# Optimization experiments

Hardware: AMD Instinct MI355X
Metric: run time of the kernel (lower is better)

## Reference

```python
import jax, jax.numpy as jnp
import numpy as np

D = 1024      # hidden_size
FF = 4096     # ff_inner_dim = 4 * D
E = 8         # num_experts
K = 2         # moe_top_k
B, L = 4, 1024


def setup_inputs() -> dict:
    key = jax.random.key(0)
    ks = jax.random.split(key, 12)
    s = 0.02  # weight init scale
    return {
        "x": jax.random.normal(ks[0], (B, L, D), jnp.float32),
        "W_gate": jax.random.normal(ks[1], (D, E), jnp.float32) * s,
        "W1": jax.random.normal(ks[2], (E, D, FF), jnp.float32) * s,
        "b1": jnp.zeros((E, FF), jnp.float32),
        "W2": jax.random.normal(ks[3], (E, FF, D), jnp.float32) * s,
        "b2": jnp.zeros((E, D), jnp.float32),
        "Ws1": jax.random.normal(ks[4], (D, FF), jnp.float32) * s,
        "bs1": jnp.zeros((FF,), jnp.float32),
        "Ws2": jax.random.normal(ks[5], (FF, D), jnp.float32) * s,
        "bs2": jnp.zeros((D,), jnp.float32),
    }


def _gelu(h):
    # torch F.gelu default = exact (erf) gelu
    return jax.nn.gelu(h, approximate=False)


def reference(x, W_gate, W1, b1, W2, b2, Ws1, bs1, Ws2, bs2):
    Bx, Lx, Dx = x.shape
    xf = x.reshape(-1, Dx)                       # [T, D]
    logits = xf @ W_gate                         # [T, E]
    probs = jax.nn.softmax(logits, axis=-1)
    top_v, top_i = jax.lax.top_k(probs, K)       # [T, K]
    top_v = top_v / jnp.sum(top_v, axis=-1, keepdims=True)
    # dense combine weights: [T, E], zero for unselected experts
    combine = jnp.sum(jax.nn.one_hot(top_i, E, dtype=xf.dtype) * top_v[..., None], axis=1)

    out = jnp.zeros_like(xf)
    for e in range(E):  # fixed small expert loop, unrolled under jit
        h = _gelu(xf @ W1[e] + b1[e])            # [T, FF]
        out = out + combine[:, e:e + 1] * (h @ W2[e] + b2[e])

    shared = _gelu(xf @ Ws1 + bs1) @ Ws2 + bs2   # [T, D]
    return (out + shared).reshape(Bx, Lx, Dx)
```

## Files before the change

kernel.cpp:

```cpp
#include <hip/hip_runtime.h>
#include <hip/hip_bf16.h>

typedef unsigned short ushort_t;
typedef __attribute__((ext_vector_type(4))) float f32x4;
typedef __attribute__((ext_vector_type(8))) short bf16x8;
typedef __attribute__((ext_vector_type(8))) unsigned short us8;

#define T_TOK 4096
#define D_DIM 1024
#define FF_DIM 4096
#define NE 8
#define ESTRIDE 4194304L

__device__ __forceinline__ unsigned short f2bf(float f) {
  __hip_bfloat16 h = __float2bfloat16(f);
  return __builtin_bit_cast(unsigned short, h);
}
__device__ __forceinline__ float gelu_f(float v) {
  return 0.5f * v * (1.0f + erff(v * 0.70710678118654752440f));
}

__global__ void gate_kernel(const float* __restrict__ x, const float* __restrict__ Wg,
                            int* __restrict__ cnt, int* __restrict__ tok,
                            float* __restrict__ wof, int* __restrict__ rankof) {
  const int t = blockIdx.x;
  const int lane = threadIdx.x;
  const float* xr = x + (long)t * D_DIM;
  float acc[NE];
#pragma unroll
  for (int e = 0; e < NE; e++) acc[e] = 0.f;
#pragma unroll
  for (int i = 0; i < 16; i++) {
    int d = i * 64 + lane;
    float xv = xr[d];
    const float* wr = Wg + d * NE;
#pragma unroll
    for (int e = 0; e < NE; e++) acc[e] += xv * wr[e];
  }
#pragma unroll
  for (int off = 32; off > 0; off >>= 1) {
#pragma unroll
    for (int e = 0; e < NE; e++) acc[e] += __shfl_xor(acc[e], off, 64);
  }
  if (lane == 0) {
    int i0 = 0;
#pragma unroll
    for (int e = 1; e < NE; e++) if (acc[e] > acc[i0]) i0 = e;
    int i1 = -1;
#pragma unroll
    for (int e = 0; e < NE; e++) {
      if (e == i0) continue;
      if (i1 < 0 || acc[e] > acc[i1]) i1 = e;
    }
    float e1 = expf(acc[i1] - acc[i0]);
    float w0 = 1.f / (1.f + e1);
    float w1 = e1 * w0;
    int s0 = atomicAdd(&cnt[i0], 1);
    tok[i0 * T_TOK + s0] = t; wof[i0 * T_TOK + s0] = w0; rankof[i0 * T_TOK + s0] = 0;
    int s1 = atomicAdd(&cnt[i1], 1);
    tok[i1 * T_TOK + s1] = t; wof[i1 * T_TOK + s1] = w1; rankof[i1 * T_TOK + s1] = 1;
    tok[8 * T_TOK + t] = t; wof[8 * T_TOK + t] = 1.f; rankof[8 * T_TOK + t] = 0;
  }
}

__global__ void scan_kernel(int* cnt, int* base) {
  if (threadIdx.x == 0 && blockIdx.x == 0) {
    int s = 0;
    for (int e = 0; e < NE; e++) { base[e] = s; s += cnt[e]; }
    base[8] = s;
    cnt[8] = T_TOK;
  }
}

__global__ void build_queue_kernel(const int* __restrict__ cnt,
                                   unsigned int* __restrict__ q1,
                                   unsigned int* __restrict__ q2,
                                   int* __restrict__ nq) {
  const int e = blockIdx.x;
  int off1 = 0, off2 = 0, tot1 = 0, tot2 = 0, M = 0;
  for (int i = 0; i < 9; i++) {
    int c = (i == 8) ? T_TOK : cnt[i];
    int m = (c + 255) >> 8;
    if (i < e) { off1 += m * 16; off2 += m * 4; }
    if (i == e) M = m;
    tot1 += m * 16; tot2 += m * 4;
  }
  for (int i = threadIdx.x; i < M * 16; i += 256) {
    int my = i >> 4, nx = i & 15;
    int ms = my >> 1, mi = my & 1, ns = nx >> 2, ni = nx & 3;
    int h = M - ms * 2; if (h > 2) h = 2;
    int pos = ms * 32 + ns * (h * 4) + mi * 4 + ni;
    q1[off1 + pos] = ((unsigned)e << 16) | ((unsigned)my << 8) | (unsigned)nx;
  }
  for (int i = threadIdx.x; i < M * 4; i += 256) {
    int my = i >> 2, nx = i & 3;
    int pos = nx * M + my;
    q2[off2 + pos] = ((unsigned)e << 16) | ((unsigned)my << 8) | (unsigned)nx;
  }
  if (e == 0 && threadIdx.x == 0) { nq[0] = tot1; nq[1] = tot2; }
}

__global__ void cvt_x_kernel(const float* __restrict__ src, ushort_t* __restrict__ dst) {
  long i = ((long)blockIdx.x * 256 + threadIdx.x) * 8;
  float4 v0 = *(const float4*)(src + i);
  float4 v1 = *(const float4*)(src + i + 4);
  us8 o;
  o[0] = f2bf(v0.x); o[1] = f2bf(v0.y); o[2] = f2bf(v0.z); o[3] = f2bf(v0.w);
  o[4] = f2bf(v1.x); o[5] = f2bf(v1.y); o[6] = f2bf(v1.z); o[7] = f2bf(v1.w);
  *(us8*)(dst + i) = o;
}

__global__ void tcvt_kernel(const float* __restrict__ W, const float* __restrict__ Wsh,
                            ushort_t* __restrict__ dst, int R, int C) {
  const float* src = (blockIdx.z == 8) ? Wsh : (W + (long)blockIdx.z * R * C);
  ushort_t* d = dst + (long)blockIdx.z * R * C;
  const int r0 = blockIdx.y * 128, c0 = blockIdx.x * 64;
  __shared__ ushort_t tile[64][136];
  const int t = threadIdx.x;
#pragma unroll
  for (int i = 0; i < 8; i++) {
    int lin = t + i * 256;
    int r = lin >> 4;
    int c = (lin & 15) * 4;
    float4 v = *(const float4*)(src + (long)(r0 + r) * C + c0 + c);
    tile[c + 0][r] = f2bf(v.x);
    tile[c + 1][r] = f2bf(v.y);
    tile[c + 2][r] = f2bf(v.z);
    tile[c + 3][r] = f2bf(v.w);
  }
  __syncthreads();
#pragma unroll
  for (int i = 0; i < 4; i++) {
    int lin = t + i * 256;
    int cc = lin >> 4, rp = lin & 15;
    us8 v = *(const us8*)&tile[cc][rp * 8];
    *(us8*)(d + (long)(c0 + cc) * R + r0 + rp * 8) = v;
  }
}

template <int K, int N, int PHASE>
__global__ __launch_bounds__(1024, 1) void gemm_kernel(
    const ushort_t* __restrict__ Abase, const ushort_t* __restrict__ WT,
    const float* __restrict__ bias_e, const float* __restrict__ bias_s,
    const int* __restrict__ cnt, const int* __restrict__ base,
    const int* __restrict__ tok, const float* __restrict__ wof,
    const int* __restrict__ rankof,
    const unsigned int* __restrict__ q, const int* __restrict__ nq_all,
    ushort_t* __restrict__ He, float* __restrict__ ybuf, float* __restrict__ out) {
  const int nq = nq_all[PHASE - 1];
  const int tid = threadIdx.x;
  const int w = tid >> 6, lane = tid & 63;
  const int wm = w >> 2, wn = w & 3;
  const int lr = lane & 15, lg = lane >> 4;

  __shared__ ushort_t lds_u[2 * 16384];
  char* const lds = (char*)lds_u;

  const int srow = tid >> 2;
  const int cg = ((tid & 3) - (srow >> 1)) & 3;

  int offA[4], offB[4];
#pragma unroll
  for (int m = 0; m < 4; m++) {
    int r = wm * 64 + m * 16 + lr;
    offA[m] = r * 64 + (((lg + (r >> 1)) & 3) << 4);
  }
#pragma unroll
  for (int n = 0; n < 4; n++) {
    int r = wn * 64 + n * 16 + lr;
    offB[n] = r * 64 + (((lg + (r >> 1)) & 3) << 4);
  }

  constexpr int NT = K / 32;
  const int chunk = gridDim.x >> 3;
  const int vbid = (blockIdx.x & 7) * chunk + (blockIdx.x >> 3);

#define STAGE(buf_, kk_)                                                        \
  do {                                                                          \
    char* dd_ = lds + (buf_) * 32768 + tid * 16;                                \
    __builtin_amdgcn_global_load_lds(                                           \
        (const __attribute__((address_space(1))) void*)(pA + (kk_)),            \
        (__attribute__((address_space(3))) void*)(dd_), 16, 0, 0);              \
    __builtin_amdgcn_global_load_lds(                                           \
        (const __attribute__((address_space(1))) void*)(pB + (kk_)),            \
        (__attribute__((address_space(3))) void*)(dd_ + 16384), 16, 0, 0);      \
  } while (0)

  for (int it = vbid; it < nq; it += gridDim.x) {
    const unsigned int item = q[it];
    const int e = item >> 16;
    const int m0 = ((item >> 8) & 0xff) * 256;
    const int n0 = (item & 0xff) * 256;
    const int count = cnt[e];

    int rr = m0 + srow;
    int rc = (rr < count) ? rr : 0;
    long arow;
    if (PHASE == 1) arow = tok[e * T_TOK + rc];
    else            arow = (long)base[e] + rc;
    const ushort_t* pA = Abase + arow * (long)K + cg * 8;
    const ushort_t* pB = WT + (long)e * ESTRIDE + (long)(n0 + srow) * K + cg * 8;

    f32x4 acc[4][4] = {};

    __builtin_amdgcn_s_barrier();
    asm volatile("" ::: "memory");
    STAGE(0, 0);

    for (int t = 0; t < NT; t++) {
      if (t + 1 < NT) {
        STAGE((t + 1) & 1, (t + 1) * 32);
        asm volatile("s_waitcnt vmcnt(2)" ::: "memory");
      } else {
        asm volatile("s_waitcnt vmcnt(0)" ::: "memory");
      }
      __builtin_amdgcn_s_barrier();
      asm volatile("" ::: "memory");

      const char* aB = lds + (t & 1) * 32768;
      const char* bB = aB + 16384;
      bf16x8 av[4], bv[4];
#pragma unroll
      for (int m = 0; m < 4; m++) av[m] = *(const bf16x8*)(aB + offA[m]);
#pragma unroll
      for (int n = 0; n < 4; n++) bv[n] = *(const bf16x8*)(bB + offB[n]);
#pragma unroll
      for (int m = 0; m < 4; m++)
#pragma unroll
        for (int n = 0; n < 4; n++)
          acc[m][n] = __builtin_amdgcn_mfma_f32_16x16x32_bf16(av[m], bv[n], acc[m][n], 0, 0, 0);

      __builtin_amdgcn_s_barrier();
      asm volatile("" ::: "memory");
    }

    const float* bias = (e == NE) ? bias_s : (bias_e + (long)e * N);
#pragma unroll
    for (int m = 0; m < 4; m++) {
#pragma unroll
      for (int j = 0; j < 4; j++) {
        int rloc = wm * 64 + m * 16 + lg * 4 + j;
        int rrr = m0 + rloc;
        if (rrr >= count) continue;
        if (PHASE == 1) {
          long orow = (long)base[e] + rrr;
#pragma unroll
          for (int n = 0; n < 4; n++) {
            int col = n0 + wn * 64 + n * 16 + lr;
            float v = acc[m][n][j] + bias[col];
            He[orow * FF_DIM + col] = f2bf(gelu_f(v));
          }
        } else {
          int tt = tok[e * T_TOK + rrr];
          if (e == NE) {
#pragma unroll
            for (int n = 0; n < 4; n++) {
              int col = n0 + wn * 64 + n * 16 + lr;
              out[(long)tt * D_DIM + col] = acc[m][n][j] + bias[col];
            }
          } else {
            float wgt = wof[e * T_TOK + rrr];
            int rk = rankof[e * T_TOK + rrr];
            float* dst = ybuf + (long)rk * ((long)T_TOK * D_DIM) + (long)tt * D_DIM;
#pragma unroll
            for (int n = 0; n < 4; n++) {
              int col = n0 + wn * 64 + n * 16 + lr;
              dst[col] = wgt * (acc[m][n][j] + bias[col]);
            }
          }
        }
      }
    }
  }
#undef STAGE
}

__global__ void final_add_kernel(float* __restrict__ out, const float* __restrict__ ybuf) {
  long i = ((long)blockIdx.x * 256 + threadIdx.x) * 4;
  float4 a = *(const float4*)(out + i);
  float4 b = *(const float4*)(ybuf + i);
  float4 c = *(const float4*)(ybuf + (long)T_TOK * D_DIM + i);
  a.x += b.x + c.x; a.y += b.y + c.y; a.z += b.z + c.z; a.w += b.w + c.w;
  *(float4*)(out + i) = a;
}

extern "C" void kernel_launch(void* const* d_in, const int* in_sizes, int n_in,
                              void* d_out, int out_size, void* d_ws, size_t ws_size,
                              hipStream_t stream) {
  (void)in_sizes; (void)n_in; (void)out_size; (void)ws_size;
  const float* x   = (const float*)d_in[0];
  const float* Wg  = (const float*)d_in[1];
  const float* W1  = (const float*)d_in[2];
  const float* b1  = (const float*)d_in[3];
  const float* W2  = (const float*)d_in[4];
  const float* b2  = (const float*)d_in[5];
  const float* Ws1 = (const float*)d_in[6];
  const float* bs1 = (const float*)d_in[7];
  const float* Ws2 = (const float*)d_in[8];
  const float* bs2 = (const float*)d_in[9];
  float* out = (float*)d_out;

  char* ws = (char*)d_ws;
  int*      cnt    = (int*)(ws + 0);
  int*      base   = (int*)(ws + 64);
  int*      tok    = (int*)(ws + 256);
  float*    wof    = (float*)(ws + 256 + 147456);
  int*      rankof = (int*)(ws + 256 + 2 * 147456);
  ushort_t* Xbf    = (ushort_t*)(ws + 442624);
  ushort_t* W1T    = (ushort_t*)(ws + 8831232);
  ushort_t* W2T    = (ushort_t*)(ws + 84328704);
  ushort_t* He     = (ushort_t*)(ws + 159826176);
  int*      nq     = (int*)(ws + 260489472);
  unsigned int* q1 = (unsigned int*)(ws + 260489536);
  unsigned int* q2 = (unsigned int*)(ws + 260489536 + 32768);
  float*    ybuf   = (float*)(ws + 261538048);

  hipMemsetAsync(cnt, 0, 64, stream);
  gate_kernel<<<T_TOK, 64, 0, stream>>>(x, Wg, cnt, tok, wof, rankof);
  scan_kernel<<<1, 64, 0, stream>>>(cnt, base);
  build_queue_kernel<<<9, 256, 0, stream>>>(cnt, q1, q2, nq);
  cvt_x_kernel<<<2048, 256, 0, stream>>>(x, Xbf);
  tcvt_kernel<<<dim3(64, 8, 9), 256, 0, stream>>>(W1, Ws1, W1T, 1024, 4096);
  tcvt_kernel<<<dim3(16, 32, 9), 256, 0, stream>>>(W2, Ws2, W2T, 4096, 1024);
  gemm_kernel<1024, 4096, 1><<<512, 1024, 0, stream>>>(
      Xbf, W1T, b1, bs1, cnt, base, tok, wof, rankof, q1, nq, He, ybuf, out);
  gemm_kernel<4096, 1024, 2><<<256, 1024, 0, stream>>>(
      He, W2T, b2, bs2, cnt, base, tok, wof, rankof, q2, nq, He, ybuf, out);
  final_add_kernel<<<4096, 256, 0, stream>>>(out, ybuf);
}
```

Measured before the change: 524.3 us.

## Switch MoE GEMMs to 256x128 tiles with 4 waves per block and fuse x conversion into gating

The grouped GEMM goes from 1024-thread blocks computing 256x256 tiles to 256-thread blocks (4 waves, 2 blocks per CU) computing 256x128 tiles. Each wave now holds an 8x4 MFMA accumulator set, and each thread issues several global-to-LDS loads per stage. The work queue is rebuilt for the narrower N tiles, and the phase-2 grid changes. MFMA sections are wrapped in s_setprio, and the bf16 conversion of x moves into the gate kernel, which removes one launch. The goal is more per-wave register reuse and better latency hiding through multiple resident blocks, at the cost of higher register pressure and reloading A tiles for twice as many N tiles.

Result: slower. 652.4 us (+24.4%).

```diff
diff --git a/kernel.cpp b/kernel.cpp
--- a/kernel.cpp
+++ b/kernel.cpp
@@ -22,10 +22,12 @@
 
 __global__ void gate_kernel(const float* __restrict__ x, const float* __restrict__ Wg,
                             int* __restrict__ cnt, int* __restrict__ tok,
-                            float* __restrict__ wof, int* __restrict__ rankof) {
+                            float* __restrict__ wof, int* __restrict__ rankof,
+                            ushort_t* __restrict__ Xbf) {
   const int t = blockIdx.x;
   const int lane = threadIdx.x;
   const float* xr = x + (long)t * D_DIM;
+  ushort_t* xb = Xbf + (long)t * D_DIM;
   float acc[NE];
 #pragma unroll
   for (int e = 0; e < NE; e++) acc[e] = 0.f;
@@ -33,6 +35,7 @@
   for (int i = 0; i < 16; i++) {
     int d = i * 64 + lane;
     float xv = xr[d];
+    xb[d] = f2bf(xv);
     const float* wr = Wg + d * NE;
 #pragma unroll
     for (int e = 0; e < NE; e++) acc[e] += xv * wr[e];
@@ -81,33 +84,23 @@
   for (int i = 0; i < 9; i++) {
     int c = (i == 8) ? T_TOK : cnt[i];
     int m = (c + 255) >> 8;
-    if (i < e) { off1 += m * 16; off2 += m * 4; }
+    if (i < e) { off1 += m * 32; off2 += m * 8; }
     if (i == e) M = m;
-    tot1 += m * 16; tot2 += m * 4;
-  }
-  for (int i = threadIdx.x; i < M * 16; i += 256) {
-    int my = i >> 4, nx = i & 15;
-    int ms = my >> 1, mi = my & 1, ns = nx >> 2, ni = nx & 3;
+    tot1 += m * 32; tot2 += m * 8;
+  }
+  for (int i = threadIdx.x; i < M * 32; i += 256) {
+    int my = i >> 5, nx = i & 31;
+    int ms = my >> 1, mi = my & 1, ns = nx >> 3, ni = nx & 7;
     int h = M - ms * 2; if (h > 2) h = 2;
-    int pos = ms * 32 + ns * (h * 4) + mi * 4 + ni;
+    int pos = ms * 64 + ns * (h * 8) + mi * 8 + ni;
     q1[off1 + pos] = ((unsigned)e << 16) | ((unsigned)my << 8) | (unsigned)nx;
   }
-  for (int i = threadIdx.x; i < M * 4; i += 256) {
-    int my = i >> 2, nx = i & 3;
+  for (int i = threadIdx.x; i < M * 8; i += 256) {
+    int my = i >> 3, nx = i & 7;
     int pos = nx * M + my;
     q2[off2 + pos] = ((unsigned)e << 16) | ((unsigned)my << 8) | (unsigned)nx;
   }
   if (e == 0 && threadIdx.x == 0) { nq[0] = tot1; nq[1] = tot2; }
-}
-
-__global__ void cvt_x_kernel(const float* __restrict__ src, ushort_t* __restrict__ dst) {
-  long i = ((long)blockIdx.x * 256 + threadIdx.x) * 8;
-  float4 v0 = *(const float4*)(src + i);
-  float4 v1 = *(const float4*)(src + i + 4);
-  us8 o;
-  o[0] = f2bf(v0.x); o[1] = f2bf(v0.y); o[2] = f2bf(v0.z); o[3] = f2bf(v0.w);
-  o[4] = f2bf(v1.x); o[5] = f2bf(v1.y); o[6] = f2bf(v1.z); o[7] = f2bf(v1.w);
-  *(us8*)(dst + i) = o;
 }
 
 __global__ void tcvt_kernel(const float* __restrict__ W, const float* __restrict__ Wsh,
@@ -139,7 +132,7 @@
 }
 
 template <int K, int N, int PHASE>
-__global__ __launch_bounds__(1024, 1) void gemm_kernel(
+__global__ __launch_bounds__(256, 2) void gemm_kernel(
     const ushort_t* __restrict__ Abase, const ushort_t* __restrict__ WT,
     const float* __restrict__ bias_e, const float* __restrict__ bias_s,
     const int* __restrict__ cnt, const int* __restrict__ base,
@@ -150,19 +143,19 @@
   const int nq = nq_all[PHASE - 1];
   const int tid = threadIdx.x;
   const int w = tid >> 6, lane = tid & 63;
-  const int wm = w >> 2, wn = w & 3;
+  const int wm = w >> 1, wn = w & 1;
   const int lr = lane & 15, lg = lane >> 4;
 
-  __shared__ ushort_t lds_u[2 * 16384];
+  __shared__ ushort_t lds_u[2 * 12288];
   char* const lds = (char*)lds_u;
 
   const int srow = tid >> 2;
   const int cg = ((tid & 3) - (srow >> 1)) & 3;
 
-  int offA[4], offB[4];
-#pragma unroll
-  for (int m = 0; m < 4; m++) {
-    int r = wm * 64 + m * 16 + lr;
+  int offA[8], offB[4];
+#pragma unroll
+  for (int m = 0; m < 8; m++) {
+    int r = wm * 128 + m * 16 + lr;
     offA[m] = r * 64 + (((lg + (r >> 1)) & 3) << 4);
   }
 #pragma unroll
@@ -177,31 +170,43 @@
 
 #define STAGE(buf_, kk_)                                                        \
   do {                                                                          \
-    char* dd_ = lds + (buf_) * 32768 + tid * 16;                                \
-    __builtin_amdgcn_global_load_lds(                                           \
-        (const __attribute__((address_space(1))) void*)(pA + (kk_)),            \
-        (__attribute__((address_space(3))) void*)(dd_), 16, 0, 0);              \
-    __builtin_amdgcn_global_load_lds(                                           \
-        (const __attribute__((address_space(1))) void*)(pB + (kk_)),            \
-        (__attribute__((address_space(3))) void*)(dd_ + 16384), 16, 0, 0);      \
+    char* dd_ = lds + (buf_) * 24576 + tid * 16;                                \
+    _Pragma("unroll")                                                           \
+    for (int i_ = 0; i_ < 4; i_++)                                              \
+      __builtin_amdgcn_global_load_lds(                                         \
+          (const __attribute__((address_space(1))) void*)(pA[i_] + (kk_)),      \
+          (__attribute__((address_space(3))) void*)(dd_ + i_ * 4096), 16, 0, 0);\
+    _Pragma("unroll")                                                           \
+    for (int i_ = 0; i_ < 2; i_++)                                              \
+      __builtin_amdgcn_global_load_lds(                                         \
+          (const __attribute__((address_space(1))) void*)(pB[i_] + (kk_)),      \
+          (__attribute__((address_space(3))) void*)(dd_ + 16384 + i_ * 4096),   \
+          16, 0, 0);                                                            \
   } while (0)
 
   for (int it = vbid; it < nq; it += gridDim.x) {
     const unsigned int item = q[it];
     const int e = item >> 16;
     const int m0 = ((item >> 8) & 0xff) * 256;
-    const int n0 = (item & 0xff) * 256;
+    const int n0 = (item & 0xff) * 128;
     const int count = cnt[e];
 
-    int rr = m0 + srow;
-    int rc = (rr < count) ? rr : 0;
-    long arow;
-    if (PHASE == 1) arow = tok[e * T_TOK + rc];
-    else            arow = (long)base[e] + rc;
-    const ushort_t* pA = Abase + arow * (long)K + cg * 8;
-    const ushort_t* pB = WT + (long)e * ESTRIDE + (long)(n0 + srow) * K + cg * 8;
-
-    f32x4 acc[4][4] = {};
+    const ushort_t* pA[4];
+    const ushort_t* pB[2];
+#pragma unroll
+    for (int i = 0; i < 4; i++) {
+      int rr = m0 + i * 64 + srow;
+      int rc = (rr < count) ? rr : 0;
+      long arow;
+      if (PHASE == 1) arow = tok[e * T_TOK + rc];
+      else            arow = (long)base[e] + rc;
+      pA[i] = Abase + arow * (long)K + cg * 8;
+    }
+#pragma unroll
+    for (int i = 0; i < 2; i++)
+      pB[i] = WT + (long)e * ESTRIDE + (long)(n0 + i * 64 + srow) * K + cg * 8;
+
+    f32x4 acc[8][4] = {};
 
     __builtin_amdgcn_s_barrier();
     asm volatile("" ::: "memory");
@@ -210,25 +215,27 @@
     for (int t = 0; t < NT; t++) {
       if (t + 1 < NT) {
         STAGE((t + 1) & 1, (t + 1) * 32);
-        asm volatile("s_waitcnt vmcnt(2)" ::: "memory");
+        asm volatile("s_waitcnt vmcnt(6)" ::: "memory");
       } else {
         asm volatile("s_waitcnt vmcnt(0)" ::: "memory");
       }
       __builtin_amdgcn_s_barrier();
       asm volatile("" ::: "memory");
 
-      const char* aB = lds + (t & 1) * 32768;
+      const char* aB = lds + (t & 1) * 24576;
       const char* bB = aB + 16384;
-      bf16x8 av[4], bv[4];
-#pragma unroll
-      for (int m = 0; m < 4; m++) av[m] = *(const bf16x8*)(aB + offA[m]);
+      bf16x8 av[8], bv[4];
+#pragma unroll
+      for (int m = 0; m < 8; m++) av[m] = *(const bf16x8*)(aB + offA[m]);
 #pragma unroll
       for (int n = 0; n < 4; n++) bv[n] = *(const bf16x8*)(bB + offB[n]);
-#pragma unroll
-      for (int m = 0; m < 4; m++)
+      __builtin_amdgcn_s_setprio(1);
+#pragma unroll
+      for (int m = 0; m < 8; m++)
 #pragma unroll
         for (int n = 0; n < 4; n++)
           acc[m][n] = __builtin_amdgcn_mfma_f32_16x16x32_bf16(av[m], bv[n], acc[m][n], 0, 0, 0);
+      __builtin_amdgcn_s_setprio(0);
 
       __builtin_amdgcn_s_barrier();
       asm volatile("" ::: "memory");
@@ -236,10 +243,10 @@
 
     const float* bias = (e == NE) ? bias_s : (bias_e + (long)e * N);
 #pragma unroll
-    for (int m = 0; m < 4; m++) {
+    for (int m = 0; m < 8; m++) {
 #pragma unroll
       for (int j = 0; j < 4; j++) {
-        int rloc = wm * 64 + m * 16 + lg * 4 + j;
+        int rloc = wm * 128 + m * 16 + lg * 4 + j;
         int rrr = m0 + rloc;
         if (rrr >= count) continue;
         if (PHASE == 1) {
@@ -316,15 +323,14 @@
   float*    ybuf   = (float*)(ws + 261538048);
 
   hipMemsetAsync(cnt, 0, 64, stream);
-  gate_kernel<<<T_TOK, 64, 0, stream>>>(x, Wg, cnt, tok, wof, rankof);
+  gate_kernel<<<T_TOK, 64, 0, stream>>>(x, Wg, cnt, tok, wof, rankof, Xbf);
   scan_kernel<<<1, 64, 0, stream>>>(cnt, base);
   build_queue_kernel<<<9, 256, 0, stream>>>(cnt, q1, q2, nq);
-  cvt_x_kernel<<<2048, 256, 0, stream>>>(x, Xbf);
   tcvt_kernel<<<dim3(64, 8, 9), 256, 0, stream>>>(W1, Ws1, W1T, 1024, 4096);
   tcvt_kernel<<<dim3(16, 32, 9), 256, 0, stream>>>(W2, Ws2, W2T, 4096, 1024);
-  gemm_kernel<1024, 4096, 1><<<512, 1024, 0, stream>>>(
+  gemm_kernel<1024, 4096, 1><<<512, 256, 0, stream>>>(
       Xbf, W1T, b1, bs1, cnt, base, tok, wof, rankof, q1, nq, He, ybuf, out);
-  gemm_kernel<4096, 1024, 2><<<256, 1024, 0, stream>>>(
+  gemm_kernel<4096, 1024, 2><<<392, 256, 0, stream>>>(
       He, W2T, b2, bs2, cnt, base, tok, wof, rankof, q2, nq, He, ybuf, out);
   final_add_kernel<<<4096, 256, 0, stream>>>(out, ybuf);
 }
```

## Fuse gate/X/W1 conversion and overlap W2 transpose with first GEMM; bf16 partials

Applied to the files above, without the earlier changes.

Merges the gate, x-to-bf16 and W1 transpose-convert kernels into one launch with interleaved block roles. The W2 transpose-convert is folded into the phase-1 GEMM launch, using 3 of every 4 blocks, so it can overlap with the GEMM compute. The per-rank expert partial outputs are stored as bf16 instead of fp32, halving that write and read traffic in the final add. Risks include extra bf16 rounding on the expert outputs and block-role imbalance or scheduling interference inside the fused GEMM launch.

After: 811.2 us. +54.7%, slower.

```diff
diff --git a/kernel.cpp b/kernel.cpp
--- a/kernel.cpp
+++ b/kernel.cpp
@@ -16,50 +16,93 @@
   __hip_bfloat16 h = __float2bfloat16(f);
   return __builtin_bit_cast(unsigned short, h);
 }
+__device__ __forceinline__ float bf2f(ushort_t u) {
+  unsigned int x = ((unsigned int)u) << 16;
+  return __builtin_bit_cast(float, x);
+}
 __device__ __forceinline__ float gelu_f(float v) {
   return 0.5f * v * (1.0f + erff(v * 0.70710678118654752440f));
 }
 
-__global__ void gate_kernel(const float* __restrict__ x, const float* __restrict__ Wg,
-                            int* __restrict__ cnt, int* __restrict__ tok,
-                            float* __restrict__ wof, int* __restrict__ rankof) {
-  const int t = blockIdx.x;
-  const int lane = threadIdx.x;
-  const float* xr = x + (long)t * D_DIM;
-  float acc[NE];
-#pragma unroll
-  for (int e = 0; e < NE; e++) acc[e] = 0.f;
+__global__ __launch_bounds__(256) void pre_kernel(
+    const float* __restrict__ x, const float* __restrict__ Wg,
+    const float* __restrict__ W1, const float* __restrict__ Ws1,
+    int* __restrict__ cnt, int* __restrict__ tok,
+    float* __restrict__ wof, int* __restrict__ rankof,
+    ushort_t* __restrict__ Xbf, ushort_t* __restrict__ W1T) {
+  __shared__ ushort_t tile[128][136];
+  const int bid = blockIdx.x, tid = threadIdx.x;
+
+  if ((bid & 3) == 0) {
+    int g = bid >> 2;
+    if (g >= 1024) return;
+    const int t = g * 4 + (tid >> 6);
+    const int lane = tid & 63;
+    const float* xr = x + (long)t * D_DIM;
+    ushort_t* xb = Xbf + (long)t * D_DIM;
+    float acc[NE];
+#pragma unroll
+    for (int e = 0; e < NE; e++) acc[e] = 0.f;
+#pragma unroll
+    for (int i = 0; i < 16; i++) {
+      int d = i * 64 + lane;
+      float xv = xr[d];
+      xb[d] = f2bf(xv);
+      const float* wr = Wg + d * NE;
+#pragma unroll
+      for (int e = 0; e < NE; e++) acc[e] += xv * wr[e];
+    }
+#pragma unroll
+    for (int off = 32; off > 0; off >>= 1) {
+#pragma unroll
+      for (int e = 0; e < NE; e++) acc[e] += __shfl_xor(acc[e], off, 64);
+    }
+    if (lane == 0) {
+      int i0 = 0;
+#pragma unroll
+      for (int e = 1; e < NE; e++) if (acc[e] > acc[i0]) i0 = e;
+      int i1 = -1;
+#pragma unroll
+      for (int e = 0; e < NE; e++) {
+        if (e == i0) continue;
+        if (i1 < 0 || acc[e] > acc[i1]) i1 = e;
+      }
+      float e1 = expf(acc[i1] - acc[i0]);
+      float w0 = 1.f / (1.f + e1);
+      float w1 = e1 * w0;
+      int s0 = atomicAdd(&cnt[i0], 1);
+      tok[i0 * T_TOK + s0] = t; wof[i0 * T_TOK + s0] = w0; rankof[i0 * T_TOK + s0] = 0;
+      int s1 = atomicAdd(&cnt[i1], 1);
+      tok[i1 * T_TOK + s1] = t; wof[i1 * T_TOK + s1] = w1; rankof[i1 * T_TOK + s1] = 1;
+      tok[8 * T_TOK + t] = t; wof[8 * T_TOK + t] = 1.f; rankof[8 * T_TOK + t] = 0;
+    }
+    return;
+  }
+
+  int tix = bid - (bid >> 2) - 1;
+  if (tix >= 2304) return;
+  const int e = tix >> 8;
+  const int rem = tix & 255;
+  const int r0 = (rem >> 5) * 128, c0 = (rem & 31) * 128;
+  const float* src = (e == 8) ? Ws1 : (W1 + (long)e * 4194304);
+  ushort_t* d = W1T + (long)e * ESTRIDE;
 #pragma unroll
   for (int i = 0; i < 16; i++) {
-    int d = i * 64 + lane;
-    float xv = xr[d];
-    const float* wr = Wg + d * NE;
-#pragma unroll
-    for (int e = 0; e < NE; e++) acc[e] += xv * wr[e];
-  }
-#pragma unroll
-  for (int off = 32; off > 0; off >>= 1) {
-#pragma unroll
-    for (int e = 0; e < NE; e++) acc[e] += __shfl_xor(acc[e], off, 64);
-  }
-  if (lane == 0) {
-    int i0 = 0;
-#pragma unroll
-    for (int e = 1; e < NE; e++) if (acc[e] > acc[i0]) i0 = e;
-    int i1 = -1;
-#pragma unroll
-    for (int e = 0; e < NE; e++) {
-      if (e == i0) continue;
-      if (i1 < 0 || acc[e] > acc[i1]) i1 = e;
-    }
-    float e1 = expf(acc[i1] - acc[i0]);
-    float w0 = 1.f / (1.f + e1);
-    float w1 = e1 * w0;
-    int s0 = atomicAdd(&cnt[i0], 1);
-    tok[i0 * T_TOK + s0] = t; wof[i0 * T_TOK + s0] = w0; rankof[i0 * T_TOK + s0] = 0;
-    int s1 = atomicAdd(&cnt[i1], 1);
-    tok[i1 * T_TOK + s1] = t; wof[i1 * T_TOK + s1] = w1; rankof[i1 * T_TOK + s1] = 1;
-    tok[8 * T_TOK + t] = t; wof[8 * T_TOK + t] = 1.f; rankof[8 * T_TOK + t] = 0;
+    int lin = tid + i * 256;
+    int r = lin >> 5, c = (lin & 31) * 4;
+    float4 v = *(const float4*)(src + (long)(r0 + r) * 4096 + c0 + c);
+    tile[c + 0][r] = f2bf(v.x);
+    tile[c + 1][r] = f2bf(v.y);
+    tile[c + 2][r] = f2bf(v.z);
+    tile[c + 3][r] = f2bf(v.w);
+  }
+  __syncthreads();
+#pragma unroll
+  for (int i = 0; i < 8; i++) {
+    int lin = tid + i * 256;
+    int cc = lin >> 4, rp = lin & 15;
+    us8 v = *(const us8*)&tile[cc][rp * 8];
+    *(us8*)(d + (long)(c0 + cc) * 1024 + r0 + rp * 8) = v;
   }
 }
 
@@ -100,45 +143,7 @@
   if (e == 0 && threadIdx.x == 0) { nq[0] = tot1; nq[1] = tot2; }
 }
 
-__global__ void cvt_x_kernel(const float* __restrict__ src, ushort_t* __restrict__ dst) {
-  long i = ((long)blockIdx.x * 256 + threadIdx.x) * 8;
-  float4 v0 = *(const float4*)(src + i);
-  float4 v1 = *(const float4*)(src + i + 4);
-  us8 o;
-  o[0] = f2bf(v0.x); o[1] = f2bf(v0.y); o[2] = f2bf(v0.z); o[3] = f2bf(v0.w);
-  o[4] = f2bf(v1.x); o[5] = f2bf(v1.y); o[6] = f2bf(v1.z); o[7] = f2bf(v1.w);
-  *(us8*)(dst + i) = o;
-}
-
-__global__ void tcvt_kernel(const float* __restrict__ W, const float* __restrict__ Wsh,
-                            ushort_t* __restrict__ dst, int R, int C) {
-  const float* src = (blockIdx.z == 8) ? Wsh : (W + (long)blockIdx.z * R * C);
-  ushort_t* d = dst + (long)blockIdx.z * R * C;
-  const int r0 = blockIdx.y * 128, c0 = blockIdx.x * 64;
-  __shared__ ushort_t tile[64][136];
-  const int t = threadIdx.x;
-#pragma unroll
-  for (int i = 0; i < 8; i++) {
-    int lin = t + i * 256;
-    int r = lin >> 4;
-    int c = (lin & 15) * 4;
-    float4 v = *(const float4*)(src + (long)(r0 + r) * C + c0 + c);
-    tile[c + 0][r] = f2bf(v.x);
-    tile[c + 1][r] = f2bf(v.y);
-    tile[c + 2][r] = f2bf(v.z);
-    tile[c + 3][r] = f2bf(v.w);
-  }
-  __syncthreads();
-#pragma unroll
-  for (int i = 0; i < 4; i++) {
-    int lin = t + i * 256;
-    int cc = lin >> 4, rp = lin & 15;
-    us8 v = *(const us8*)&tile[cc][rp * 8];
-    *(us8*)(d + (long)(c0 + cc) * R + r0 + rp * 8) = v;
-  }
-}
-
-template <int K, int N, int PHASE>
+template <int K, int N, int PHASE, bool FUSE>
 __global__ __launch_bounds__(1024, 1) void gemm_kernel(
     const ushort_t* __restrict__ Abase, const ushort_t* __restrict__ WT,
     const float* __restrict__ bias_e, const float* __restrict__ bias_s,
@@ -146,15 +151,53 @@
     const int* __restrict__ tok, const float* __restrict__ wof,
     const int* __restrict__ rankof,
     const unsigned int* __restrict__ q, const int* __restrict__ nq_all,
-    ushort_t* __restrict__ He, float* __restrict__ ybuf, float* __restrict__ out) {
+    ushort_t* __restrict__ He, ushort_t* __restrict__ ybuf, float* __restrict__ out,
+    const float* __restrict__ W2src, const float* __restrict__ Ws2src,
+    ushort_t* __restrict__ W2Tdst) {
+  __shared__ char smem[65536];
+  const int tid = threadIdx.x;
+  const int bid = blockIdx.x;
+
+  if (FUSE && (bid & 3) != 0) {
+    int tix = bid - (bid >> 2) - 1;
+    if (tix >= 2304) return;
+    const int e = tix >> 8;
+    const int rem = tix & 255;
+    const int r0 = (rem >> 3) * 128, c0 = (rem & 7) * 128;
+    const float* src = (e == 8) ? Ws2src : (W2src + (long)e * 4194304);
+    ushort_t* d = W2Tdst + (long)e * ESTRIDE;
+    ushort_t (*tile)[136] = (ushort_t (*)[136])smem;
+#pragma unroll
+    for (int i = 0; i < 4; i++) {
+      int lin = tid + i * 1024;
+      int r = lin >> 5, c = (lin & 31) * 4;
+      float4 v = *(const float4*)(src + (long)(r0 + r) * 1024 + c0 + c);
+      tile[c + 0][r] = f2bf(v.x);
+      tile[c + 1][r] = f2bf(v.y);
+      tile[c + 2][r] = f2bf(v.z);
+      tile[c + 3][r] = f2bf(v.w);
+    }
+    __syncthreads();
+#pragma unroll
+    for (int i = 0; i < 2; i++) {
+      int lin = tid + i * 1024;
+      int cc = lin >> 4, rp = lin & 15;
+      us8 v = *(const us8*)&tile[cc][rp * 8];
+      *(us8*)(d + (long)(c0 + cc) * 4096 + r0 + rp * 8) = v;
+    }
+    return;
+  }
+
+  const int NBLK = FUSE ? (int)(gridDim.x >> 2) : (int)gridDim.x;
+  const int gidx = FUSE ? (bid >> 2) : bid;
   const int nq = nq_all[PHASE - 1];
-  const int tid = threadIdx.x;
+  const int chunk = NBLK >> 3;
+  const int vbid = (gidx < (chunk << 3)) ? ((gidx & 7) * chunk + (gidx >> 3)) : gidx;
+
   const int w = tid >> 6, lane = tid & 63;
   const int wm = w >> 2, wn = w & 3;
   const int lr = lane & 15, lg = lane >> 4;
-
-  __shared__ ushort_t lds_u[2 * 16384];
-  char* const lds = (char*)lds_u;
+  char* const lds = smem;
 
   const int srow = tid >> 2;
   const int cg = ((tid & 3) - (srow >> 1)) & 3;
@@ -172,8 +215,6 @@
   }
 
   constexpr int NT = K / 32;
-  const int chunk = gridDim.x >> 3;
-  const int vbid = (blockIdx.x & 7) * chunk + (blockIdx.x >> 3);
 
 #define STAGE(buf_, kk_)                                                        \
   do {                                                                          \
@@ -186,7 +227,7 @@
         (__attribute__((address_space(3))) void*)(dd_ + 16384), 16, 0, 0);      \
   } while (0)
 
-  for (int it = vbid; it < nq; it += gridDim.x) {
+  for (int it = vbid; it < nq; it += NBLK) {
     const unsigned int item = q[it];
     const int e = item >> 16;
     const int m0 = ((item >> 8) & 0xff) * 256;
@@ -261,11 +302,11 @@
           } else {
             float wgt = wof[e * T_TOK + rrr];
             int rk = rankof[e * T_TOK + rrr];
-            float* dst = ybuf + (long)rk * ((long)T_TOK * D_DIM) + (long)tt * D_DIM;
+            ushort_t* dst = ybuf + (long)rk * ((long)T_TOK * D_DIM) + (long)tt * D_DIM;
 #pragma unroll
             for (int n = 0; n < 4; n++) {
               int col = n0 + wn * 64 + n * 16 + lr;
-              dst[col] = wgt * (acc[m][n][j] + bias[col]);
+              dst[col] = f2bf(wgt * (acc[m][n][j] + bias[col]));
             }
           }
         }
@@ -275,13 +316,19 @@
 #undef STAGE
 }
 
-__global__ void final_add_kernel(float* __restrict__ out, const float* __restrict__ ybuf) {
-  long i = ((long)blockIdx.x * 256 + threadIdx.x) * 4;
-  float4 a = *(const float4*)(out + i);
-  float4 b = *(const float4*)(ybuf + i);
-  float4 c = *(const float4*)(ybuf + (long)T_TOK * D_DIM + i);
-  a.x += b.x + c.x; a.y += b.y + c.y; a.z += b.z + c.z; a.w += b.w + c.w;
-  *(float4*)(out + i) = a;
+__global__ void final_add_kernel(float* __restrict__ out, const ushort_t* __restrict__ ybuf) {
+  long i = ((long)blockIdx.x * 256 + threadIdx.x) * 8;
+  float4 a0 = *(const float4*)(out + i);
+  float4 a1 = *(const float4*)(out + i + 4);
+  us8 b = *(const us8*)(ybuf + i);
+  us8 c = *(const us8*)(ybuf + (long)T_TOK * D_DIM + i);
+  float r[8];
+#pragma unroll
+  for (int k = 0; k < 8; k++) r[k] = bf2f(b[k]) + bf2f(c[k]);
+  a0.x += r[0]; a0.y += r[1]; a0.z += r[2]; a0.w += r[3];
+  a1.x += r[4]; a1.y += r[5]; a1.z += r[6]; a1.w += r[7];
+  *(float4*)(out + i) = a0;
+  *(float4*)(out + i + 4) = a1;
 }
 
 extern "C" void kernel_launch(void* const* d_in, const int* in_sizes, int n_in,
@@ -313,18 +360,17 @@
   int*      nq     = (int*)(ws + 260489472);
   unsigned int* q1 = (unsigned int*)(ws + 260489536);
   unsigned int* q2 = (unsigned int*)(ws + 260489536 + 32768);
-  float*    ybuf   = (float*)(ws + 261538048);
+  ushort_t* ybuf   = (ushort_t*)(ws + 261538048);
 
   hipMemsetAsync(cnt, 0, 64, stream);
-  gate_kernel<<<T_TOK, 64, 0, stream>>>(x, Wg, cnt, tok, wof, rankof);
+  pre_kernel<<<4352, 256, 0, stream>>>(x, Wg, W1, Ws1, cnt, tok, wof, rankof, Xbf, W1T);
   scan_kernel<<<1, 64, 0, stream>>>(cnt, base);
   build_queue_kernel<<<9, 256, 0, stream>>>(cnt, q1, q2, nq);
-  cvt_x_kernel<<<2048, 256, 0, stream>>>(x, Xbf);
-  tcvt_kernel<<<dim3(64, 8, 9), 256, 0, stream>>>(W1, Ws1, W1T, 1024, 4096);
-  tcvt_kernel<<<dim3(16, 32, 9), 256, 0, stream>>>(W2, Ws2, W2T, 4096, 1024);
-  gemm_kernel<1024, 4096, 1><<<512, 1024, 0, stream>>>(
-      Xbf, W1T, b1, bs1, cnt, base, tok, wof, rankof, q1, nq, He, ybuf, out);
-  gemm_kernel<4096, 1024, 2><<<256, 1024, 0, stream>>>(
-      He, W2T, b2, bs2, cnt, base, tok, wof, rankof, q2, nq, He, ybuf, out);
-  final_add_kernel<<<4096, 256, 0, stream>>>(out, ybuf);
-}
+  gemm_kernel<1024, 4096, 1, true><<<3264, 1024, 0, stream>>>(
+      Xbf, W1T, b1, bs1, cnt, base, tok, wof, rankof, q1, nq, He, ybuf, out,
+      W2, Ws2, W2T);
+  gemm_kernel<4096, 1024, 2, false><<<256, 1024, 0, stream>>>(
+      He, W2T, b2, bs2, cnt, base, tok, wof, rankof, q2, nq, He, ybuf, out,
+      nullptr, nullptr, nullptr);
+  final_add_kernel<<<2048, 256, 0, stream>>>(out, ybuf);
+}
```
